# Performance work log

Hardware: AMD Instinct MI355X
Metric: run time of the kernel (lower is better)

The kernel has to match this reference:

```python
import jax, jax.numpy as jnp
import numpy as np
import math

CHANNELS = 128
NUM_NODES = 170
LENGTH = 12
BATCH = 128


def setup_inputs() -> dict:
    key = jax.random.key(0)
    k_x, k_es = jax.random.split(key)
    x = jax.random.normal(k_x, (BATCH, CHANNELS, NUM_NODES, LENGTH), dtype=jnp.float32)
    # xavier_uniform for E_s [channels, num_nodes]
    bound = math.sqrt(6.0 / (CHANNELS + NUM_NODES))
    E_s = jax.random.uniform(k_es, (CHANNELS, NUM_NODES), dtype=jnp.float32,
                             minval=-bound, maxval=bound)
    return {"x": x, "E_s": E_s}


def reference(x, E_s):
    # x: [B, C, N, T], E_s: [C, M] with M == N (num_nodes)
    # Note: the original also computes E_t = x * E_tod**2, which is dead code
    # (never used in the returned value), so it is omitted here.
    C = x.shape[1]
    # node embeddings: sum over channel and time -> [B, N, M]
    E_d = jnp.tanh(jnp.einsum('bcnt,cm->bnm', x, E_s))
    # node-node similarity: contract over the M (embedding) axis -> [B, N, N]
    scores = jax.nn.relu(jnp.einsum('bnm,bkm->bnk', E_d, E_d) / jnp.sqrt(jnp.float32(C)))
    A_adp = jax.nn.softmax(scores, axis=-1)  # [B, N, N]
    A_mean = A_adp.mean(axis=0)              # [N, N]
    return (A_mean > 0.5).astype(jnp.float32)
```

## Files before the change

### kernel.cpp

```cpp
#include <hip/hip_runtime.h>
#include <math.h>

#define NB 128
#define NC 128
#define NN 170
#define NT 12
#define MP 176
#define MEST 192

#define EST_SZ ((size_t)MEST * NC)
#define XS_SZ  ((size_t)NB * NC * NN)
#define ED_SZ  ((size_t)NB * NN * MP)
#define P_SZ   ((size_t)NB * NN * MP)

typedef _Float16 h8 __attribute__((ext_vector_type(8)));
typedef _Float16 h4 __attribute__((ext_vector_type(4)));
typedef __fp16   g2 __attribute__((ext_vector_type(2)));
typedef float    f4 __attribute__((ext_vector_type(4)));

__device__ __forceinline__ float fast_tanh(float x) {
    float cx = fminf(fmaxf(x, -15.f), 15.f);
    float e  = __expf(2.f * cx);
    return (e - 1.f) * __builtin_amdgcn_rcpf(e + 1.f);
}

__global__ __launch_bounds__(256) void k0t_transpose_es(const float* __restrict__ Es,
                                                        _Float16* __restrict__ Est) {
    int idx = blockIdx.x * 256 + threadIdx.x;
    if (idx >= MEST * NC) return;
    int m = idx >> 7, c = idx & 127;
    Est[idx] = (m < NN) ? (_Float16)Es[c * NN + m] : (_Float16)0.f;
}

__global__ __launch_bounds__(256) void k1_tsum(const float* __restrict__ x,
                                               _Float16* __restrict__ xs) {
    unsigned tid = blockIdx.x * 256 + threadIdx.x;
    unsigned bc = tid / 85u;
    unsigned p  = tid - bc * 85u;
    const float4* q = reinterpret_cast<const float4*>(
        x + (size_t)bc * (NN * NT) + (size_t)p * (2 * NT));
    float4 f0 = q[0], f1 = q[1], f2 = q[2];
    float4 f3 = q[3], f4v = q[4], f5 = q[5];
    float s0 = ((f0.x + f0.y) + (f0.z + f0.w))
             + ((f1.x + f1.y) + (f1.z + f1.w))
             + ((f2.x + f2.y) + (f2.z + f2.w));
    float s1 = ((f3.x + f3.y) + (f3.z + f3.w))
             + ((f4v.x + f4v.y) + (f4v.z + f4v.w))
             + ((f5.x + f5.y) + (f5.z + f5.w));
    g2 pk = __builtin_amdgcn_cvt_pkrtz(s0, s1);
    *reinterpret_cast<g2*>(xs + (size_t)bc * NN + 2 * p) = pk;
}

__global__ __launch_bounds__(256) void k2_ed_mfma(const _Float16* __restrict__ xs,
                                                  const _Float16* __restrict__ Est,
                                                  _Float16* __restrict__ Ed) {
    const int b = blockIdx.y, n0 = blockIdx.x * 32;
    const int t = threadIdx.x;
    const int lane = t & 63, wave = t >> 6;
    const int l15 = lane & 15, quad = lane >> 4;

    __shared__ __align__(16) _Float16 At[32 * 40];

    const _Float16* __restrict__ xsb = xs + (size_t)b * NC * NN;

    f4 acc[2][3] = {};
    for (int c0 = 0; c0 < NC; c0 += 32) {
        __syncthreads();
        #pragma unroll
        for (int it = 0; it < 4; ++it) {
            int slot = t + it * 256;
            int c = slot >> 5, n = slot & 31;
            _Float16 v = (_Float16)0.f;
            if (n0 + n < NN)
                v = xsb[(size_t)(c0 + c) * NN + n0 + n];
            At[n * 40 + c] = v;
        }
        __syncthreads();
        const int ko = quad * 8;
        h8 a0 = *reinterpret_cast<const h8*>(&At[l15 * 40 + ko]);
        h8 a1 = *reinterpret_cast<const h8*>(&At[(16 + l15) * 40 + ko]);
        #pragma unroll
        for (int ci = 0; ci < 3; ++ci) {
            int kc = (wave * 3 + ci) * 16 + l15;
            h8 bf = *reinterpret_cast<const h8*>(Est + (size_t)kc * NC + c0 + ko);
            acc[0][ci] = __builtin_amdgcn_mfma_f32_16x16x32_f16(a0, bf, acc[0][ci], 0, 0, 0);
            acc[1][ci] = __builtin_amdgcn_mfma_f32_16x16x32_f16(a1, bf, acc[1][ci], 0, 0, 0);
        }
    }

    #pragma unroll
    for (int rt = 0; rt < 2; ++rt)
        #pragma unroll
        for (int ci = 0; ci < 3; ++ci) {
            int m = (wave * 3 + ci) * 16 + l15;
            if (m >= MP) continue;
            #pragma unroll
            for (int reg = 0; reg < 4; ++reg) {
                int n = n0 + rt * 16 + quad * 4 + reg;
                if (n >= NN) continue;
                Ed[((size_t)(b * NN + n)) * MP + m] = (_Float16)fast_tanh(acc[rt][ci][reg]);
            }
        }
}

__global__ __launch_bounds__(256) void k3_scores_mfma(const _Float16* __restrict__ Ed,
                                                      _Float16* __restrict__ P) {
    const int b = blockIdx.y, r0 = blockIdx.x * 32;
    const int t = threadIdx.x;
    const int lane = t & 63, wave = t >> 6;
    const int l15 = lane & 15, quad = lane >> 4;

    __shared__ __align__(16) _Float16 Eh[192 * 40];
    __shared__ __align__(16) float    Sc[32 * 204];

    const _Float16* __restrict__ Edb = Ed + (size_t)b * NN * MP;

    f4 acc[2][3] = {};
    for (int mc = 0; mc < 192; mc += 32) {
        __syncthreads();
        #pragma unroll
        for (int it = 0; it < 3; ++it) {
            int idx = t + it * 256;
            int row = idx >> 2, q = idx & 3;
            int col = mc + q * 8;
            h8 v = {};
            if (row < NN && col < MP)
                v = *reinterpret_cast<const h8*>(Edb + (size_t)row * MP + col);
            *reinterpret_cast<h8*>(&Eh[row * 40 + q * 8]) = v;
        }
        __syncthreads();
        const int ko = quad * 8;
        h8 a0 = *reinterpret_cast<const h8*>(&Eh[(r0 + l15) * 40 + ko]);
        h8 a1 = *reinterpret_cast<const h8*>(&Eh[(r0 + 16 + l15) * 40 + ko]);
        #pragma unroll
        for (int ci = 0; ci < 3; ++ci) {
            int kc = (wave * 3 + ci) * 16 + l15;
            h8 bf = *reinterpret_cast<const h8*>(&Eh[kc * 40 + ko]);
            acc[0][ci] = __builtin_amdgcn_mfma_f32_16x16x32_f16(a0, bf, acc[0][ci], 0, 0, 0);
            acc[1][ci] = __builtin_amdgcn_mfma_f32_16x16x32_f16(a1, bf, acc[1][ci], 0, 0, 0);
        }
    }

    const float scale = 0.08838834764831845f;
    #pragma unroll
    for (int rt = 0; rt < 2; ++rt)
        #pragma unroll
        for (int ci = 0; ci < 3; ++ci) {
            int col = (wave * 3 + ci) * 16 + l15;
            #pragma unroll
            for (int reg = 0; reg < 4; ++reg) {
                int rloc = rt * 16 + quad * 4 + reg;
                Sc[rloc * 204 + col] = fmaxf(acc[rt][ci][reg] * scale, 0.f);
            }
        }
    __syncthreads();

    for (int rr = 0; rr < 8; ++rr) {
        int r = wave * 8 + rr;
        int n = r0 + r;
        if (n >= NN) continue;
        float v0 = Sc[r * 204 + lane];
        float v1 = Sc[r * 204 + lane + 64];
        int  k2i = lane + 128;
        bool has2 = (k2i < NN);
        float v2 = has2 ? Sc[r * 204 + k2i] : -1.f;
        float m = fmaxf(fmaxf(v0, v1), v2);
        #pragma unroll
        for (int off = 32; off; off >>= 1) m = fmaxf(m, __shfl_xor(m, off, 64));
        float e0 = __expf(v0 - m);
        float e1 = __expf(v1 - m);
        float e2 = has2 ? __expf(v2 - m) : 0.f;
        float s = e0 + e1 + e2;
        #pragma unroll
        for (int off = 32; off; off >>= 1) s += __shfl_xor(s, off, 64);
        float inv = 1.f / s;
        _Float16* Pr = P + ((size_t)(b * NN + n)) * MP;
        Pr[lane]      = (_Float16)(e0 * inv);
        Pr[lane + 64] = (_Float16)(e1 * inv);
        if (has2) Pr[k2i] = (_Float16)(e2 * inv);
    }
}

__global__ __launch_bounds__(256) void k4_mean_thresh(const _Float16* __restrict__ P,
                                                      float* __restrict__ out) {
    int p = blockIdx.x * 256 + threadIdx.x;
    if (p >= NN * NN) return;
    int n = p / NN, k = p - n * NN;
    const _Float16* base = P + (size_t)n * MP + k;
    float s0 = 0.f, s1 = 0.f, s2 = 0.f, s3 = 0.f;
    #pragma unroll
    for (int b = 0; b < NB; b += 4) {
        s0 += (float)base[(size_t)(b + 0) * NN * MP];
        s1 += (float)base[(size_t)(b + 1) * NN * MP];
        s2 += (float)base[(size_t)(b + 2) * NN * MP];
        s3 += (float)base[(size_t)(b + 3) * NN * MP];
    }
    float s = (s0 + s1) + (s2 + s3);
    out[p] = (s * (1.f / 128.f) > 0.5f) ? 1.f : 0.f;
}

extern "C" void kernel_launch(void* const* d_in, const int* in_sizes, int n_in,
                              void* d_out, int out_size, void* d_ws, size_t ws_size,
                              hipStream_t stream) {
    const float* x  = (const float*)d_in[0];
    const float* Es = (const float*)d_in[1];
    float* out = (float*)d_out;

    _Float16* Est = (_Float16*)d_ws;
    _Float16* xs  = Est + EST_SZ;
    _Float16* Ed  = xs + XS_SZ;
    _Float16* P   = Ed + ED_SZ;

    k0t_transpose_es<<<96, 256, 0, stream>>>(Es, Est);
    k1_tsum<<<5440, 256, 0, stream>>>(x, xs);
    k2_ed_mfma<<<dim3(6, 128), 256, 0, stream>>>(xs, Est, Ed);
    k3_scores_mfma<<<dim3(6, 128), 256, 0, stream>>>(Ed, P);
    k4_mean_thresh<<<113, 256, 0, stream>>>(P, out);
}
```

Before: 225.1 us.

## Fuse embedding GEMM with score/softmax kernel, keep Ed in LDS

Merges the Es transpose into the time-sum kernel, and fuses the Ed GEMM+tanh with the score GEMM and softmax so that Ed stays in shared memory with XOR-swizzled layouts instead of a global round trip. The xs buffer is padded to a stride of 176 so each batch can be loaded with vector reads. Each block now handles a full batch's Ed, split over 2 row-halves, so Ed is computed twice per batch. The grid drops to 256 blocks and uses about 120KB of LDS per block, which cuts occupancy and parallelism.

```diff
diff --git a/kernel.cpp b/kernel.cpp
--- a/kernel.cpp
+++ b/kernel.cpp
@@ -6,15 +6,14 @@
 #define NN 170
 #define NT 12
 #define MP 176
+#define XSTR 176
 #define MEST 192
 
 #define EST_SZ ((size_t)MEST * NC)
-#define XS_SZ  ((size_t)NB * NC * NN)
-#define ED_SZ  ((size_t)NB * NN * MP)
+#define XS_SZ  ((size_t)NB * NC * XSTR)
 #define P_SZ   ((size_t)NB * NN * MP)
 
 typedef _Float16 h8 __attribute__((ext_vector_type(8)));
-typedef _Float16 h4 __attribute__((ext_vector_type(4)));
 typedef __fp16   g2 __attribute__((ext_vector_type(2)));
 typedef float    f4 __attribute__((ext_vector_type(4)));
 
@@ -24,160 +23,175 @@
     return (e - 1.f) * __builtin_amdgcn_rcpf(e + 1.f);
 }
 
-__global__ __launch_bounds__(256) void k0t_transpose_es(const float* __restrict__ Es,
-                                                        _Float16* __restrict__ Est) {
-    int idx = blockIdx.x * 256 + threadIdx.x;
-    if (idx >= MEST * NC) return;
-    int m = idx >> 7, c = idx & 127;
-    Est[idx] = (m < NN) ? (_Float16)Es[c * NN + m] : (_Float16)0.f;
-}
-
-__global__ __launch_bounds__(256) void k1_tsum(const float* __restrict__ x,
-                                               _Float16* __restrict__ xs) {
-    unsigned tid = blockIdx.x * 256 + threadIdx.x;
-    unsigned bc = tid / 85u;
-    unsigned p  = tid - bc * 85u;
-    const float4* q = reinterpret_cast<const float4*>(
-        x + (size_t)bc * (NN * NT) + (size_t)p * (2 * NT));
-    float4 f0 = q[0], f1 = q[1], f2 = q[2];
-    float4 f3 = q[3], f4v = q[4], f5 = q[5];
-    float s0 = ((f0.x + f0.y) + (f0.z + f0.w))
-             + ((f1.x + f1.y) + (f1.z + f1.w))
-             + ((f2.x + f2.y) + (f2.z + f2.w));
-    float s1 = ((f3.x + f3.y) + (f3.z + f3.w))
-             + ((f4v.x + f4v.y) + (f4v.z + f4v.w))
-             + ((f5.x + f5.y) + (f5.z + f5.w));
-    g2 pk = __builtin_amdgcn_cvt_pkrtz(s0, s1);
-    *reinterpret_cast<g2*>(xs + (size_t)bc * NN + 2 * p) = pk;
-}
-
-__global__ __launch_bounds__(256) void k2_ed_mfma(const _Float16* __restrict__ xs,
-                                                  const _Float16* __restrict__ Est,
-                                                  _Float16* __restrict__ Ed) {
-    const int b = blockIdx.y, n0 = blockIdx.x * 32;
+__global__ __launch_bounds__(256) void k1_tsum_est(const float* __restrict__ x,
+                                                   const float* __restrict__ Es,
+                                                   _Float16* __restrict__ xs,
+                                                   _Float16* __restrict__ Est) {
+    const int bid = blockIdx.x;
+    if (bid < 5440) {
+        unsigned tid = bid * 256u + threadIdx.x;
+        unsigned bc = tid / 85u;
+        unsigned p  = tid - bc * 85u;
+        const float4* q = reinterpret_cast<const float4*>(
+            x + (size_t)bc * (NN * NT) + (size_t)p * (2 * NT));
+        float4 f0 = q[0], f1 = q[1], f2 = q[2];
+        float4 f3 = q[3], f4v = q[4], f5 = q[5];
+        float s0 = ((f0.x + f0.y) + (f0.z + f0.w))
+                 + ((f1.x + f1.y) + (f1.z + f1.w))
+                 + ((f2.x + f2.y) + (f2.z + f2.w));
+        float s1 = ((f3.x + f3.y) + (f3.z + f3.w))
+                 + ((f4v.x + f4v.y) + (f4v.z + f4v.w))
+                 + ((f5.x + f5.y) + (f5.z + f5.w));
+        g2 pk = __builtin_amdgcn_cvt_pkrtz(s0, s1);
+        *reinterpret_cast<g2*>(xs + (size_t)bc * XSTR + 2 * p) = pk;
+        if (p < 3)
+            *reinterpret_cast<unsigned*>(xs + (size_t)bc * XSTR + 170 + 2 * p) = 0u;
+    } else {
+        int idx = (bid - 5440) * 256 + threadIdx.x;
+        int m = idx >> 7, c = idx & 127;
+        Est[idx] = (m < NN) ? (_Float16)Es[c * NN + m] : (_Float16)0.f;
+    }
+}
+
+#define ATSW(row, c)  ((row) * 128 + (((((c) >> 3) ^ ((row) & 7)) << 3) | ((c) & 7)))
+#define EDSW(row, m)  ((row) * 192 + (((((m) >> 3) ^ ((row) & 7)) << 3) | ((m) & 7)))
+#define SCSTR 204
+
+__global__ __launch_bounds__(256) void k23_fused(const _Float16* __restrict__ xs,
+                                                 const _Float16* __restrict__ Est,
+                                                 _Float16* __restrict__ P) {
+    const int h = blockIdx.x, b = blockIdx.y;
     const int t = threadIdx.x;
     const int lane = t & 63, wave = t >> 6;
     const int l15 = lane & 15, quad = lane >> 4;
-
-    __shared__ __align__(16) _Float16 At[32 * 40];
-
-    const _Float16* __restrict__ xsb = xs + (size_t)b * NC * NN;
-
-    f4 acc[2][3] = {};
-    for (int c0 = 0; c0 < NC; c0 += 32) {
+    const int r0 = h * 96;
+
+    __shared__ __align__(16) _Float16 EdL[192 * 192];
+    __shared__ __align__(16) char UN[192 * 128 * 2];
+    _Float16* At = (_Float16*)UN;
+    float*    Sc = (float*)UN;
+
+    const _Float16* __restrict__ xsb = xs + (size_t)b * NC * XSTR;
+    #pragma unroll
+    for (int it = 0; it < 12; ++it) {
+        int g  = t + it * 256;
+        int gg = g >> 7;
+        int c  = g & 127;
+        int n0g = gg * 8;
+        h8 v = {};
+        if (n0g < XSTR)
+            v = *reinterpret_cast<const h8*>(xsb + (size_t)c * XSTR + n0g);
+        #pragma unroll
+        for (int j = 0; j < 8; ++j)
+            At[ATSW(n0g + j, c)] = v[j];
+    }
+    __syncthreads();
+
+    {
+        h8 a[3][4];
+        #pragma unroll
+        for (int rt = 0; rt < 3; ++rt)
+            #pragma unroll
+            for (int kk = 0; kk < 4; ++kk) {
+                int row = wave * 48 + rt * 16 + l15;
+                int cg  = kk * 4 + quad;
+                a[rt][kk] = *reinterpret_cast<const h8*>(
+                    &At[row * 128 + ((cg ^ (row & 7)) << 3)]);
+            }
+        #pragma unroll 2
+        for (int ct = 0; ct < 12; ++ct) {
+            h8 bfr[4];
+            #pragma unroll
+            for (int kk = 0; kk < 4; ++kk)
+                bfr[kk] = *reinterpret_cast<const h8*>(
+                    Est + (size_t)(ct * 16 + l15) * NC + kk * 32 + quad * 8);
+            f4 acc1[3] = {};
+            #pragma unroll
+            for (int kk = 0; kk < 4; ++kk)
+                #pragma unroll
+                for (int rt = 0; rt < 3; ++rt)
+                    acc1[rt] = __builtin_amdgcn_mfma_f32_16x16x32_f16(
+                        a[rt][kk], bfr[kk], acc1[rt], 0, 0, 0);
+            #pragma unroll
+            for (int rt = 0; rt < 3; ++rt)
+                #pragma unroll
+                for (int reg = 0; reg < 4; ++reg) {
+                    int n = wave * 48 + rt * 16 + quad * 4 + reg;
+                    int m = ct * 16 + l15;
+                    EdL[EDSW(n, m)] = (_Float16)fast_tanh(acc1[rt][reg]);
+                }
+        }
+    }
+    __syncthreads();
+
+    f4 acc2[6][3] = {};
+    #pragma unroll
+    for (int mc = 0; mc < 192; mc += 32) {
+        h8 a2[6], b2[3];
+        #pragma unroll
+        for (int rt = 0; rt < 6; ++rt) {
+            int row = r0 + rt * 16 + l15;
+            int mg  = (mc >> 3) + quad;
+            a2[rt] = *reinterpret_cast<const h8*>(
+                &EdL[row * 192 + ((mg ^ (row & 7)) << 3)]);
+        }
+        #pragma unroll
+        for (int ci = 0; ci < 3; ++ci) {
+            int row = (wave * 3 + ci) * 16 + l15;
+            int mg  = (mc >> 3) + quad;
+            b2[ci] = *reinterpret_cast<const h8*>(
+                &EdL[row * 192 + ((mg ^ (row & 7)) << 3)]);
+        }
+        #pragma unroll
+        for (int rt = 0; rt < 6; ++rt)
+            #pragma unroll
+            for (int ci = 0; ci < 3; ++ci)
+                acc2[rt][ci] = __builtin_amdgcn_mfma_f32_16x16x32_f16(
+                    a2[rt], b2[ci], acc2[rt][ci], 0, 0, 0);
+    }
+
+    const float scale = 0.08838834764831845f;
+    #pragma unroll
+    for (int p = 0; p < 2; ++p) {
         __syncthreads();
         #pragma unroll
-        for (int it = 0; it < 4; ++it) {
-            int slot = t + it * 256;
-            int c = slot >> 5, n = slot & 31;
-            _Float16 v = (_Float16)0.f;
-            if (n0 + n < NN)
-                v = xsb[(size_t)(c0 + c) * NN + n0 + n];
-            At[n * 40 + c] = v;
+        for (int rt3 = 0; rt3 < 3; ++rt3) {
+            int rt = p * 3 + rt3;
+            #pragma unroll
+            for (int ci = 0; ci < 3; ++ci) {
+                int col = (wave * 3 + ci) * 16 + l15;
+                #pragma unroll
+                for (int reg = 0; reg < 4; ++reg) {
+                    int rloc = rt3 * 16 + quad * 4 + reg;
+                    Sc[rloc * SCSTR + col] = fmaxf(acc2[rt][ci][reg] * scale, 0.f);
+                }
+            }
         }
         __syncthreads();
-        const int ko = quad * 8;
-        h8 a0 = *reinterpret_cast<const h8*>(&At[l15 * 40 + ko]);
-        h8 a1 = *reinterpret_cast<const h8*>(&At[(16 + l15) * 40 + ko]);
-        #pragma unroll
-        for (int ci = 0; ci < 3; ++ci) {
-            int kc = (wave * 3 + ci) * 16 + l15;
-            h8 bf = *reinterpret_cast<const h8*>(Est + (size_t)kc * NC + c0 + ko);
-            acc[0][ci] = __builtin_amdgcn_mfma_f32_16x16x32_f16(a0, bf, acc[0][ci], 0, 0, 0);
-            acc[1][ci] = __builtin_amdgcn_mfma_f32_16x16x32_f16(a1, bf, acc[1][ci], 0, 0, 0);
-        }
-    }
-
-    #pragma unroll
-    for (int rt = 0; rt < 2; ++rt)
-        #pragma unroll
-        for (int ci = 0; ci < 3; ++ci) {
-            int m = (wave * 3 + ci) * 16 + l15;
-            if (m >= MP) continue;
-            #pragma unroll
-            for (int reg = 0; reg < 4; ++reg) {
-                int n = n0 + rt * 16 + quad * 4 + reg;
-                if (n >= NN) continue;
-                Ed[((size_t)(b * NN + n)) * MP + m] = (_Float16)fast_tanh(acc[rt][ci][reg]);
-            }
-        }
-}
-
-__global__ __launch_bounds__(256) void k3_scores_mfma(const _Float16* __restrict__ Ed,
-                                                      _Float16* __restrict__ P) {
-    const int b = blockIdx.y, r0 = blockIdx.x * 32;
-    const int t = threadIdx.x;
-    const int lane = t & 63, wave = t >> 6;
-    const int l15 = lane & 15, quad = lane >> 4;
-
-    __shared__ __align__(16) _Float16 Eh[192 * 40];
-    __shared__ __align__(16) float    Sc[32 * 204];
-
-    const _Float16* __restrict__ Edb = Ed + (size_t)b * NN * MP;
-
-    f4 acc[2][3] = {};
-    for (int mc = 0; mc < 192; mc += 32) {
-        __syncthreads();
-        #pragma unroll
-        for (int it = 0; it < 3; ++it) {
-            int idx = t + it * 256;
-            int row = idx >> 2, q = idx & 3;
-            int col = mc + q * 8;
-            h8 v = {};
-            if (row < NN && col < MP)
-                v = *reinterpret_cast<const h8*>(Edb + (size_t)row * MP + col);
-            *reinterpret_cast<h8*>(&Eh[row * 40 + q * 8]) = v;
-        }
-        __syncthreads();
-        const int ko = quad * 8;
-        h8 a0 = *reinterpret_cast<const h8*>(&Eh[(r0 + l15) * 40 + ko]);
-        h8 a1 = *reinterpret_cast<const h8*>(&Eh[(r0 + 16 + l15) * 40 + ko]);
-        #pragma unroll
-        for (int ci = 0; ci < 3; ++ci) {
-            int kc = (wave * 3 + ci) * 16 + l15;
-            h8 bf = *reinterpret_cast<const h8*>(&Eh[kc * 40 + ko]);
-            acc[0][ci] = __builtin_amdgcn_mfma_f32_16x16x32_f16(a0, bf, acc[0][ci], 0, 0, 0);
-            acc[1][ci] = __builtin_amdgcn_mfma_f32_16x16x32_f16(a1, bf, acc[1][ci], 0, 0, 0);
-        }
-    }
-
-    const float scale = 0.08838834764831845f;
-    #pragma unroll
-    for (int rt = 0; rt < 2; ++rt)
-        #pragma unroll
-        for (int ci = 0; ci < 3; ++ci) {
-            int col = (wave * 3 + ci) * 16 + l15;
-            #pragma unroll
-            for (int reg = 0; reg < 4; ++reg) {
-                int rloc = rt * 16 + quad * 4 + reg;
-                Sc[rloc * 204 + col] = fmaxf(acc[rt][ci][reg] * scale, 0.f);
-            }
-        }
-    __syncthreads();
-
-    for (int rr = 0; rr < 8; ++rr) {
-        int r = wave * 8 + rr;
-        int n = r0 + r;
-        if (n >= NN) continue;
-        float v0 = Sc[r * 204 + lane];
-        float v1 = Sc[r * 204 + lane + 64];
-        int  k2i = lane + 128;
-        bool has2 = (k2i < NN);
-        float v2 = has2 ? Sc[r * 204 + k2i] : -1.f;
-        float m = fmaxf(fmaxf(v0, v1), v2);
-        #pragma unroll
-        for (int off = 32; off; off >>= 1) m = fmaxf(m, __shfl_xor(m, off, 64));
-        float e0 = __expf(v0 - m);
-        float e1 = __expf(v1 - m);
-        float e2 = has2 ? __expf(v2 - m) : 0.f;
-        float s = e0 + e1 + e2;
-        #pragma unroll
-        for (int off = 32; off; off >>= 1) s += __shfl_xor(s, off, 64);
-        float inv = 1.f / s;
-        _Float16* Pr = P + ((size_t)(b * NN + n)) * MP;
-        Pr[lane]      = (_Float16)(e0 * inv);
-        Pr[lane + 64] = (_Float16)(e1 * inv);
-        if (has2) Pr[k2i] = (_Float16)(e2 * inv);
+        for (int rr = 0; rr < 12; ++rr) {
+            int r = wave * 12 + rr;
+            int n = r0 + p * 48 + r;
+            if (n >= NN) continue;
+            float v0 = Sc[r * SCSTR + lane];
+            float v1 = Sc[r * SCSTR + lane + 64];
+            int  k2i = lane + 128;
+            bool has2 = (k2i < NN);
+            float v2 = has2 ? Sc[r * SCSTR + k2i] : -1.f;
+            float m = fmaxf(fmaxf(v0, v1), v2);
+            #pragma unroll
+            for (int off = 32; off; off >>= 1) m = fmaxf(m, __shfl_xor(m, off, 64));
+            float e0 = __expf(v0 - m);
+            float e1 = __expf(v1 - m);
+            float e2 = has2 ? __expf(v2 - m) : 0.f;
+            float s = e0 + e1 + e2;
+            #pragma unroll
+            for (int off = 32; off; off >>= 1) s += __shfl_xor(s, off, 64);
+            float inv = 1.f / s;
+            _Float16* Pr = P + ((size_t)(b * NN + n)) * MP;
+            Pr[lane]      = (_Float16)(e0 * inv);
+            Pr[lane + 64] = (_Float16)(e1 * inv);
+            if (has2) Pr[k2i] = (_Float16)(e2 * inv);
+        }
     }
 }
 
@@ -208,12 +222,9 @@
 
     _Float16* Est = (_Float16*)d_ws;
     _Float16* xs  = Est + EST_SZ;
-    _Float16* Ed  = xs + XS_SZ;
-    _Float16* P   = Ed + ED_SZ;
-
-    k0t_transpose_es<<<96, 256, 0, stream>>>(Es, Est);
-    k1_tsum<<<5440, 256, 0, stream>>>(x, xs);
-    k2_ed_mfma<<<dim3(6, 128), 256, 0, stream>>>(xs, Est, Ed);
-    k3_scores_mfma<<<dim3(6, 128), 256, 0, stream>>>(Ed, P);
+    _Float16* P   = xs + XS_SZ;
+
+    k1_tsum_est<<<5536, 256, 0, stream>>>(x, Es, xs, Est);
+    k23_fused<<<dim3(2, 128), 256, 0, stream>>>(xs, Est, P);
     k4_mean_thresh<<<113, 256, 0, stream>>>(P, out);
 }
```

After: 227.3 us. About the same (+1.0%).

## Fuse E_s transpose into time-sum and drop LDS staging in GEMMs

Applied to the files above, without the earlier changes.

Folds the E_s transpose into the time-sum kernel, which removes one launch. The time-sum now reads x with coalesced float4 loads through shared memory and writes a node-major [b][n][c] layout padded to 192 nodes. With that layout, and Ed padded to 192x192, both MFMA kernels load operands straight from global memory, with no LDS staging or block barriers in the K loop. Padded rows of xst are never written, so they hold uninitialised workspace data; the results stay valid only because those rows and columns are discarded later.

```diff
diff --git a/kernel.cpp b/kernel.cpp
--- a/kernel.cpp
+++ b/kernel.cpp
@@ -5,17 +5,16 @@
 #define NC 128
 #define NN 170
 #define NT 12
+#define NP 192
 #define MP 176
 #define MEST 192
 
 #define EST_SZ ((size_t)MEST * NC)
-#define XS_SZ  ((size_t)NB * NC * NN)
-#define ED_SZ  ((size_t)NB * NN * MP)
+#define XST_SZ ((size_t)NB * NP * NC)
+#define ED_SZ  ((size_t)NB * NP * NP)
 #define P_SZ   ((size_t)NB * NN * MP)
 
 typedef _Float16 h8 __attribute__((ext_vector_type(8)));
-typedef _Float16 h4 __attribute__((ext_vector_type(4)));
-typedef __fp16   g2 __attribute__((ext_vector_type(2)));
 typedef float    f4 __attribute__((ext_vector_type(4)));
 
 __device__ __forceinline__ float fast_tanh(float x) {
@@ -24,34 +23,42 @@
     return (e - 1.f) * __builtin_amdgcn_rcpf(e + 1.f);
 }
 
-__global__ __launch_bounds__(256) void k0t_transpose_es(const float* __restrict__ Es,
-                                                        _Float16* __restrict__ Est) {
-    int idx = blockIdx.x * 256 + threadIdx.x;
-    if (idx >= MEST * NC) return;
-    int m = idx >> 7, c = idx & 127;
-    Est[idx] = (m < NN) ? (_Float16)Es[c * NN + m] : (_Float16)0.f;
-}
-
-__global__ __launch_bounds__(256) void k1_tsum(const float* __restrict__ x,
-                                               _Float16* __restrict__ xs) {
-    unsigned tid = blockIdx.x * 256 + threadIdx.x;
-    unsigned bc = tid / 85u;
-    unsigned p  = tid - bc * 85u;
-    const float4* q = reinterpret_cast<const float4*>(
-        x + (size_t)bc * (NN * NT) + (size_t)p * (2 * NT));
-    float4 f0 = q[0], f1 = q[1], f2 = q[2];
-    float4 f3 = q[3], f4v = q[4], f5 = q[5];
-    float s0 = ((f0.x + f0.y) + (f0.z + f0.w))
-             + ((f1.x + f1.y) + (f1.z + f1.w))
-             + ((f2.x + f2.y) + (f2.z + f2.w));
-    float s1 = ((f3.x + f3.y) + (f3.z + f3.w))
-             + ((f4v.x + f4v.y) + (f4v.z + f4v.w))
-             + ((f5.x + f5.y) + (f5.z + f5.w));
-    g2 pk = __builtin_amdgcn_cvt_pkrtz(s0, s1);
-    *reinterpret_cast<g2*>(xs + (size_t)bc * NN + 2 * p) = pk;
-}
-
-__global__ __launch_bounds__(256) void k2_ed_mfma(const _Float16* __restrict__ xs,
+__global__ __launch_bounds__(256) void k1_tsum_est(const float* __restrict__ x,
+                                                   const float* __restrict__ Es,
+                                                   _Float16* __restrict__ xst,
+                                                   _Float16* __restrict__ Est) {
+    const int bid = blockIdx.x;
+    const int t = threadIdx.x;
+    if (bid < 2048) {
+        const int b = bid >> 4, c0 = (bid & 15) * 8;
+        __shared__ float L[8][512];
+        const float4* xq = reinterpret_cast<const float4*>(
+            x + ((size_t)(b * NC + c0)) * (NN * NT));
+        #pragma unroll
+        for (int it = 0; it < 16; ++it) {
+            int s = t + it * 256;
+            if (s < 4080) {
+                float4 v = xq[s];
+                int c = s / 510, r = s - c * 510;
+                L[c][r] = (v.x + v.y) + (v.z + v.w);
+            }
+        }
+        __syncthreads();
+        if (t < NN) {
+            h8 o;
+            #pragma unroll
+            for (int c = 0; c < 8; ++c)
+                o[c] = (_Float16)(L[c][3 * t] + L[c][3 * t + 1] + L[c][3 * t + 2]);
+            *reinterpret_cast<h8*>(xst + ((size_t)b * NP + t) * NC + c0) = o;
+        }
+    } else {
+        int idx = (bid - 2048) * 256 + t;
+        int m = idx >> 7, c = idx & 127;
+        Est[idx] = (m < NN) ? (_Float16)Es[c * NN + m] : (_Float16)0.f;
+    }
+}
+
+__global__ __launch_bounds__(256) void k2_ed_mfma(const _Float16* __restrict__ xst,
                                                   const _Float16* __restrict__ Est,
                                                   _Float16* __restrict__ Ed) {
     const int b = blockIdx.y, n0 = blockIdx.x * 32;
@@ -59,49 +66,36 @@
     const int lane = t & 63, wave = t >> 6;
     const int l15 = lane & 15, quad = lane >> 4;
 
-    __shared__ __align__(16) _Float16 At[32 * 40];
-
-    const _Float16* __restrict__ xsb = xs + (size_t)b * NC * NN;
+    const _Float16* __restrict__ xb = xst + (size_t)b * NP * NC;
 
     f4 acc[2][3] = {};
-    for (int c0 = 0; c0 < NC; c0 += 32) {
-        __syncthreads();
-        #pragma unroll
-        for (int it = 0; it < 4; ++it) {
-            int slot = t + it * 256;
-            int c = slot >> 5, n = slot & 31;
-            _Float16 v = (_Float16)0.f;
-            if (n0 + n < NN)
-                v = xsb[(size_t)(c0 + c) * NN + n0 + n];
-            At[n * 40 + c] = v;
-        }
-        __syncthreads();
-        const int ko = quad * 8;
-        h8 a0 = *reinterpret_cast<const h8*>(&At[l15 * 40 + ko]);
-        h8 a1 = *reinterpret_cast<const h8*>(&At[(16 + l15) * 40 + ko]);
-        #pragma unroll
-        for (int ci = 0; ci < 3; ++ci) {
-            int kc = (wave * 3 + ci) * 16 + l15;
-            h8 bf = *reinterpret_cast<const h8*>(Est + (size_t)kc * NC + c0 + ko);
+    #pragma unroll
+    for (int kk = 0; kk < 4; ++kk) {
+        int ks = kk * 32 + quad * 8;
+        h8 a0 = *reinterpret_cast<const h8*>(xb + (size_t)(n0 + l15) * NC + ks);
+        h8 a1 = *reinterpret_cast<const h8*>(xb + (size_t)(n0 + 16 + l15) * NC + ks);
+        #pragma unroll
+        for (int ci = 0; ci < 3; ++ci) {
+            int m = (wave * 3 + ci) * 16 + l15;
+            h8 bf = *reinterpret_cast<const h8*>(Est + (size_t)m * NC + ks);
             acc[0][ci] = __builtin_amdgcn_mfma_f32_16x16x32_f16(a0, bf, acc[0][ci], 0, 0, 0);
             acc[1][ci] = __builtin_amdgcn_mfma_f32_16x16x32_f16(a1, bf, acc[1][ci], 0, 0, 0);
         }
     }
-
     #pragma unroll
     for (int rt = 0; rt < 2; ++rt)
         #pragma unroll
         for (int ci = 0; ci < 3; ++ci) {
             int m = (wave * 3 + ci) * 16 + l15;
-            if (m >= MP) continue;
             #pragma unroll
             for (int reg = 0; reg < 4; ++reg) {
                 int n = n0 + rt * 16 + quad * 4 + reg;
-                if (n >= NN) continue;
-                Ed[((size_t)(b * NN + n)) * MP + m] = (_Float16)fast_tanh(acc[rt][ci][reg]);
+                Ed[((size_t)b * NP + n) * NP + m] = (_Float16)fast_tanh(acc[rt][ci][reg]);
             }
         }
 }
+
+#define SCSTR 204
 
 __global__ __launch_bounds__(256) void k3_scores_mfma(const _Float16* __restrict__ Ed,
                                                       _Float16* __restrict__ P) {
@@ -110,32 +104,20 @@
     const int lane = t & 63, wave = t >> 6;
     const int l15 = lane & 15, quad = lane >> 4;
 
-    __shared__ __align__(16) _Float16 Eh[192 * 40];
-    __shared__ __align__(16) float    Sc[32 * 204];
-
-    const _Float16* __restrict__ Edb = Ed + (size_t)b * NN * MP;
+    __shared__ __align__(16) float Sc[32 * SCSTR];
+
+    const _Float16* __restrict__ Eb = Ed + (size_t)b * NP * NP;
 
     f4 acc[2][3] = {};
+    #pragma unroll 2
     for (int mc = 0; mc < 192; mc += 32) {
-        __syncthreads();
-        #pragma unroll
-        for (int it = 0; it < 3; ++it) {
-            int idx = t + it * 256;
-            int row = idx >> 2, q = idx & 3;
-            int col = mc + q * 8;
-            h8 v = {};
-            if (row < NN && col < MP)
-                v = *reinterpret_cast<const h8*>(Edb + (size_t)row * MP + col);
-            *reinterpret_cast<h8*>(&Eh[row * 40 + q * 8]) = v;
-        }
-        __syncthreads();
-        const int ko = quad * 8;
-        h8 a0 = *reinterpret_cast<const h8*>(&Eh[(r0 + l15) * 40 + ko]);
-        h8 a1 = *reinterpret_cast<const h8*>(&Eh[(r0 + 16 + l15) * 40 + ko]);
+        int ks = mc + quad * 8;
+        h8 a0 = *reinterpret_cast<const h8*>(Eb + (size_t)(r0 + l15) * NP + ks);
+        h8 a1 = *reinterpret_cast<const h8*>(Eb + (size_t)(r0 + 16 + l15) * NP + ks);
         #pragma unroll
         for (int ci = 0; ci < 3; ++ci) {
             int kc = (wave * 3 + ci) * 16 + l15;
-            h8 bf = *reinterpret_cast<const h8*>(&Eh[kc * 40 + ko]);
+            h8 bf = *reinterpret_cast<const h8*>(Eb + (size_t)kc * NP + ks);
             acc[0][ci] = __builtin_amdgcn_mfma_f32_16x16x32_f16(a0, bf, acc[0][ci], 0, 0, 0);
             acc[1][ci] = __builtin_amdgcn_mfma_f32_16x16x32_f16(a1, bf, acc[1][ci], 0, 0, 0);
         }
@@ -150,7 +132,7 @@
             #pragma unroll
             for (int reg = 0; reg < 4; ++reg) {
                 int rloc = rt * 16 + quad * 4 + reg;
-                Sc[rloc * 204 + col] = fmaxf(acc[rt][ci][reg] * scale, 0.f);
+                Sc[rloc * SCSTR + col] = fmaxf(acc[rt][ci][reg] * scale, 0.f);
             }
         }
     __syncthreads();
@@ -159,11 +141,11 @@
         int r = wave * 8 + rr;
         int n = r0 + r;
         if (n >= NN) continue;
-        float v0 = Sc[r * 204 + lane];
-        float v1 = Sc[r * 204 + lane + 64];
+        float v0 = Sc[r * SCSTR + lane];
+        float v1 = Sc[r * SCSTR + lane + 64];
         int  k2i = lane + 128;
         bool has2 = (k2i < NN);
-        float v2 = has2 ? Sc[r * 204 + k2i] : -1.f;
+        float v2 = has2 ? Sc[r * SCSTR + k2i] : -1.f;
         float m = fmaxf(fmaxf(v0, v1), v2);
         #pragma unroll
         for (int off = 32; off; off >>= 1) m = fmaxf(m, __shfl_xor(m, off, 64));
@@ -207,13 +189,12 @@
     float* out = (float*)d_out;
 
     _Float16* Est = (_Float16*)d_ws;
-    _Float16* xs  = Est + EST_SZ;
-    _Float16* Ed  = xs + XS_SZ;
+    _Float16* xst = Est + EST_SZ;
+    _Float16* Ed  = xst + XST_SZ;
     _Float16* P   = Ed + ED_SZ;
 
-    k0t_transpose_es<<<96, 256, 0, stream>>>(Es, Est);
-    k1_tsum<<<5440, 256, 0, stream>>>(x, xs);
-    k2_ed_mfma<<<dim3(6, 128), 256, 0, stream>>>(xs, Est, Ed);
+    k1_tsum_est<<<2144, 256, 0, stream>>>(x, Es, xst, Est);
+    k2_ed_mfma<<<dim3(6, 128), 256, 0, stream>>>(xst, Est, Ed);
     k3_scores_mfma<<<dim3(6, 128), 256, 0, stream>>>(Ed, P);
     k4_mean_thresh<<<113, 256, 0, stream>>>(P, out);
 }
```

Result: slower. 236.6 us (+5.1%).
